# Kernel optimization log

Measured on AMD Instinct MI355X. Metric: run time of the kernel, lower is better.

## Reference

```python
import jax, jax.numpy as jnp
import numpy as np

K_CHAINS, N_STATES, ALPHABET, SEQ_LEN = 3, 12, 32, 64


def setup_inputs() -> dict:
    key = jax.random.key(0)
    k0, k1, k2, k3, k4 = jax.random.split(key, 5)
    return {
        "ys": jax.random.randint(k0, (SEQ_LEN,), 0, ALPHABET),
        "transition": jax.random.normal(k1, (K_CHAINS, N_STATES, N_STATES), jnp.float32),
        "emission": jax.random.normal(k2, (K_CHAINS, N_STATES, ALPHABET), jnp.float32),
        "choice": jax.random.normal(k3, (K_CHAINS,), jnp.float32),
        "prior": jax.random.normal(k4, (K_CHAINS, N_STATES), jnp.float32),
    }


def reference(ys, transition, emission, choice, prior):
    K, S = transition.shape[0], transition.shape[1]
    c = jax.nn.log_softmax(choice)                  # (K,)
    t = jax.nn.log_softmax(transition, axis=-1)     # (K,S,S)
    e = jax.nn.log_softmax(emission, axis=-1)       # (K,S,A)
    p = jax.nn.log_softmax(prior, axis=-1)          # (K,S)

    # enumerate expanded state space: tuples (s_1..s_K, i) -> N = S^K * K rows
    grids = jnp.meshgrid(*([jnp.arange(S)] * K + [jnp.arange(K)]), indexing="ij")
    tbl = jnp.stack(grids, -1).reshape(-1, K + 1)   # (N, K+1)
    states = tbl[:, :K]                             # (N, K) chain states
    chain = tbl[:, K]                               # (N,)   active chain index

    # transition matrix A[m, n] = logprob(old expanded state n -> new expanded state m)
    onehot = jax.nn.one_hot(chain, K, dtype=bool)   # (N, K)
    eq = states[:, None, :] == states[None, :, :]   # (N_new, N_old, K)
    valid = jnp.where(onehot[:, None, :], True, eq).all(-1)  # non-active chains unchanged
    s_new = jnp.take_along_axis(states, chain[:, None], axis=1)[:, 0]  # (N,) new state of active chain
    s_old = states[:, chain]                        # (N_old, N_new): old state at chain[m]
    t_term = t[chain[None, :], s_old, s_new[None, :]]  # (N_old, N_new)
    Amat = c[chain][:, None] + t_term.T + jnp.where(valid, 0.0, -jnp.inf)  # (N_new, N_old)

    # emission table B[m, y] = e[chain[m], state of active chain, y]
    B = e[chain, s_new]                             # (N, A)

    # initial alpha: sum_j p[j, s_j] + c[i]
    alpha0 = p[jnp.arange(K)[None, :], states].sum(-1) + c[chain]  # (N,)

    def step(alpha, y):
        alpha = B[:, y] + jax.nn.logsumexp(alpha[None, :] + Amat, axis=-1)
        return alpha, None

    alpha, _ = jax.lax.scan(step, alpha0, ys)
    return jax.nn.logsumexp(alpha)
```

## Files before the change

kernel.cpp:

```cpp
#include <hip/hip_runtime.h>
#include <math.h>

#define KC 3
#define S 12
#define SS 1728
#define AB 32
#define TLEN 64
#define NTHREADS 448
#define NWAVES 7
#define NSLICE 432
#define LN2F 0.69314718055994530942f

__global__ __launch_bounds__(NTHREADS, 2)
void hmm_fwd_kernel(const int* __restrict__ ys,
                    const float* __restrict__ transition,
                    const float* __restrict__ emission,
                    const float* __restrict__ choice,
                    const float* __restrict__ prior,
                    float* __restrict__ out)
{
    __shared__ __align__(16) float A[2][KC][SS];
    __shared__ __align__(16) float T_s[KC][S][S];
    __shared__ float EC[KC][S][AB];
    __shared__ float p_lin[KC][S];
    __shared__ float c_lin[KC];
    __shared__ int   ys_s[TLEN];
    __shared__ float wsum[NWAVES];

    const int tid = threadIdx.x;

    if (tid < TLEN) ys_s[tid] = ys[tid];

    if (tid == 0) {
        float m = fmaxf(fmaxf(choice[0], choice[1]), choice[2]);
        float e0 = __expf(choice[0]-m), e1 = __expf(choice[1]-m), e2 = __expf(choice[2]-m);
        float inv = 1.f / (e0+e1+e2);
        c_lin[0] = e0*inv; c_lin[1] = e1*inv; c_lin[2] = e2*inv;
    }
    if (tid >= 1 && tid < 1 + KC) {
        int k = tid - 1;
        float m = -INFINITY;
        #pragma unroll
        for (int i = 0; i < S; ++i) m = fmaxf(m, prior[k*S + i]);
        float ev[S]; float s = 0.f;
        #pragma unroll
        for (int i = 0; i < S; ++i) { ev[i] = __expf(prior[k*S + i] - m); s += ev[i]; }
        float inv = 1.f / s;
        #pragma unroll
        for (int i = 0; i < S; ++i) p_lin[k][i] = ev[i] * inv;
    }
    if (tid >= 64 && tid < 64 + KC*S) {
        int r = tid - 64;
        int k = r / S, i = r % S;
        const float* row = transition + (k*S + i)*S;
        float m = -INFINITY;
        #pragma unroll
        for (int j = 0; j < S; ++j) m = fmaxf(m, row[j]);
        float ev[S]; float s = 0.f;
        #pragma unroll
        for (int j = 0; j < S; ++j) { ev[j] = __expf(row[j] - m); s += ev[j]; }
        float inv = 1.f / s;
        #pragma unroll
        for (int j = 0; j < S; ++j) T_s[k][i][j] = ev[j] * inv;
    }
    if (tid >= 128 && tid < 128 + KC*S) {
        int r = tid - 128;
        int k = r / S, si = r % S;
        float cm = fmaxf(fmaxf(choice[0], choice[1]), choice[2]);
        float ce = __expf(choice[k]-cm) /
                   (__expf(choice[0]-cm) + __expf(choice[1]-cm) + __expf(choice[2]-cm));
        const float* row = emission + (k*S + si)*AB;
        float m = -INFINITY;
        #pragma unroll
        for (int a = 0; a < AB; ++a) m = fmaxf(m, row[a]);
        float ev[AB]; float s = 0.f;
        #pragma unroll
        for (int a = 0; a < AB; ++a) { ev[a] = __expf(row[a] - m); s += ev[a]; }
        float inv = ce / s;
        #pragma unroll
        for (int a = 0; a < AB; ++a) EC[k][si][a] = ev[a] * inv;
    }
    __syncthreads();

    const bool active = (tid < NSLICE);
    const int sk = tid / 144;
    const int q  = tid % 144;
    const int ka = (sk == 0) ? 1 : 0;
    const int kb = (sk == 2) ? 1 : 2;

    int base = 0, str = 0;
    float2 T2[S][6];
    float  own[S];
    int    off[S];

    if (active) {
        if (sk == 0)      { base = q;                   str = 144; }
        else if (sk == 1) { base = (q/12)*144 + (q%12); str = 12;  }
        else              { base = q*12;                str = 1;   }
        #pragma unroll
        for (int i = 0; i < S; ++i) off[i] = base + i*str;

        #pragma unroll
        for (int i = 0; i < S; ++i) {
            const float2* tr = reinterpret_cast<const float2*>(&T_s[sk][i][0]);
            #pragma unroll
            for (int m = 0; m < 6; ++m) T2[i][m] = tr[m];
        }

        const float pq = p_lin[ka == 1 ? 1 : 0][q/12] * 0.f +
                         p_lin[(sk==0)?1:0][q/12] * p_lin[(sk==2)?1:2][q%12];
        const float ck = c_lin[sk];
        #pragma unroll
        for (int i = 0; i < S; ++i) {
            float v = p_lin[sk][i] * pq * ck;
            own[i] = v;
            A[0][sk][off[i]] = v;
        }
    }
    __syncthreads();

    float logR = 0.f;
    float invR = 1.f;
    int cur = 0;

    for (int t = 0; t < TLEN; ++t) {
        const int y = ys_s[t];

        if (active) {
            float ecol[S];
            #pragma unroll
            for (int j = 0; j < S; ++j) ecol[j] = EC[sk][j][y];

            float beta[S];
            if (sk == 2) {
                const float4* pa = reinterpret_cast<const float4*>(&A[cur][0][base]);
                const float4* pb = reinterpret_cast<const float4*>(&A[cur][1][base]);
                #pragma unroll
                for (int m = 0; m < 3; ++m) {
                    float4 x = pa[m], z = pb[m];
                    beta[4*m+0] = own[4*m+0] + x.x + z.x;
                    beta[4*m+1] = own[4*m+1] + x.y + z.y;
                    beta[4*m+2] = own[4*m+2] + x.z + z.z;
                    beta[4*m+3] = own[4*m+3] + x.w + z.w;
                }
            } else {
                #pragma unroll
                for (int i = 0; i < S; ++i)
                    beta[i] = own[i] + A[cur][ka][off[i]] + A[cur][kb][off[i]];
            }

            float2 acc2[6];
            #pragma unroll
            for (int m = 0; m < 6; ++m) { acc2[m].x = 0.f; acc2[m].y = 0.f; }
            #pragma unroll
            for (int i = 0; i < S; ++i) {
                const float bv = beta[i];
                #pragma unroll
                for (int m = 0; m < 6; ++m) {
                    acc2[m].x += bv * T2[i][m].x;
                    acc2[m].y += bv * T2[i][m].y;
                }
            }

            #pragma unroll
            for (int j = 0; j < S; ++j) {
                float a = (j & 1) ? acc2[j>>1].y : acc2[j>>1].x;
                own[j] = a * ecol[j] * invR;
            }

            if (sk == 2) {
                float4* pw = reinterpret_cast<float4*>(&A[cur^1][2][base]);
                pw[0] = make_float4(own[0], own[1], own[2],  own[3]);
                pw[1] = make_float4(own[4], own[5], own[6],  own[7]);
                pw[2] = make_float4(own[8], own[9], own[10], own[11]);
            } else {
                #pragma unroll
                for (int j = 0; j < S; ++j) A[cur^1][sk][off[j]] = own[j];
            }
        }

        if ((t & 7) == 7) {
            float part = 0.f;
            if (active) {
                #pragma unroll
                for (int j = 0; j < S; ++j) part += own[j];
            }
            #pragma unroll
            for (int o = 32; o > 0; o >>= 1) part += __shfl_xor(part, o);
            if ((tid & 63) == 0) wsum[tid >> 6] = part;
        }
        __syncthreads();

        if ((t & 7) == 7 && t < TLEN-1) {
            float R = wsum[0];
            #pragma unroll
            for (int w = 1; w < NWAVES; ++w) R += wsum[w];
            invR = __builtin_amdgcn_rcpf(R);
            logR += __log2f(R);
        } else {
            invR = 1.f;
        }
        cur ^= 1;
    }

    if (tid == 0) {
        float R = wsum[0];
        #pragma unroll
        for (int w = 1; w < NWAVES; ++w) R += wsum[w];
        out[0] = LN2F * (__log2f(R) + logR);
    }
}

extern "C" void kernel_launch(void* const* d_in, const int* in_sizes, int n_in,
                              void* d_out, int out_size, void* d_ws, size_t ws_size,
                              hipStream_t stream) {
    const int*   ys         = (const int*)  d_in[0];
    const float* transition = (const float*)d_in[1];
    const float* emission   = (const float*)d_in[2];
    const float* choice     = (const float*)d_in[3];
    const float* prior      = (const float*)d_in[4];
    float* out = (float*)d_out;

    hipLaunchKernelGGL(hmm_fwd_kernel, dim3(1), dim3(NTHREADS), 0, stream,
                       ys, transition, emission, choice, prior, out);
}
```

Baseline: 72.55 us.

## Split forward step into beta-sum phase with swizzled shared layout

Restructures each time step into two phases. First, every thread sums the three chain slices of alpha into a shared beta buffer using float4 loads. After a barrier, each slice thread gathers its beta column through an XOR-swizzled address map meant to avoid LDS bank conflicts, and the emission table is transposed so each emission column is read as three float4 loads. The intent is to cut strided scattered LDS reads and redundant per-slice summation, at the cost of an extra __syncthreads per step and a single non-double-buffered alpha array whose in-place writes must stay race-free.

```diff
diff --git a/kernel.cpp b/kernel.cpp
--- a/kernel.cpp
+++ b/kernel.cpp
@@ -11,6 +11,13 @@
 #define NSLICE 432
 #define LN2F 0.69314718055994530942f
 
+__device__ __forceinline__ int swz_word(int n) {
+    int r   = n / 12;
+    int pos = n % 12;
+    int v = (((r & 1) << 2) | (pos >> 2)) ^ ((r >> 1) & 7);
+    return ((r >> 1) << 5) + (v << 2) + (pos & 3);
+}
+
 __global__ __launch_bounds__(NTHREADS, 2)
 void hmm_fwd_kernel(const int* __restrict__ ys,
                     const float* __restrict__ transition,
@@ -19,9 +26,10 @@
                     const float* __restrict__ prior,
                     float* __restrict__ out)
 {
-    __shared__ __align__(16) float A[2][KC][SS];
-    __shared__ __align__(16) float T_s[KC][S][S];
-    __shared__ float EC[KC][S][AB];
+    __shared__ __align__(16) float ABUF[5760];
+    __shared__ __align__(16) float BETA[2304];
+    __shared__ __align__(16) float ECt[KC*AB*S];
+    __shared__ float T_s[KC][S][S];
     __shared__ float p_lin[KC][S];
     __shared__ float c_lin[KC];
     __shared__ int   ys_s[TLEN];
@@ -65,11 +73,11 @@
     }
     if (tid >= 128 && tid < 128 + KC*S) {
         int r = tid - 128;
-        int k = r / S, si = r % S;
+        int k = r / S, sj = r % S;
         float cm = fmaxf(fmaxf(choice[0], choice[1]), choice[2]);
         float ce = __expf(choice[k]-cm) /
                    (__expf(choice[0]-cm) + __expf(choice[1]-cm) + __expf(choice[2]-cm));
-        const float* row = emission + (k*S + si)*AB;
+        const float* row = emission + (k*S + sj)*AB;
         float m = -INFINITY;
         #pragma unroll
         for (int a = 0; a < AB; ++a) m = fmaxf(m, row[a]);
@@ -78,112 +86,112 @@
         for (int a = 0; a < AB; ++a) { ev[a] = __expf(row[a] - m); s += ev[a]; }
         float inv = ce / s;
         #pragma unroll
-        for (int a = 0; a < AB; ++a) EC[k][si][a] = ev[a] * inv;
+        for (int a = 0; a < AB; ++a) ECt[(k*AB + a)*S + sj] = ev[a] * inv;
     }
     __syncthreads();
 
-    const bool active = (tid < NSLICE);
+    const bool active = tid < NSLICE;
     const int sk = tid / 144;
     const int q  = tid % 144;
-    const int ka = (sk == 0) ? 1 : 0;
-    const int kb = (sk == 2) ? 1 : 2;
-
-    int base = 0, str = 0;
-    float2 T2[S][6];
-    float  own[S];
-    int    off[S];
+
+    int rd[S], wr[S];
+    float4 T4[S][3];
 
     if (active) {
-        if (sk == 0)      { base = q;                   str = 144; }
-        else if (sk == 1) { base = (q/12)*144 + (q%12); str = 12;  }
-        else              { base = q*12;                str = 1;   }
-        #pragma unroll
-        for (int i = 0; i < S; ++i) off[i] = base + i*str;
+        int n[S];
+        if (sk == 0) {
+            #pragma unroll
+            for (int j = 0; j < S; ++j) n[j] = j*144 + q;
+        } else if (sk == 1) {
+            int b = (q/12)*144 + (q%12);
+            #pragma unroll
+            for (int j = 0; j < S; ++j) n[j] = b + j*12;
+        } else {
+            #pragma unroll
+            for (int j = 0; j < S; ++j) n[j] = q*12 + j;
+        }
+        #pragma unroll
+        for (int j = 0; j < S; ++j) rd[j] = swz_word(n[j]);
+        #pragma unroll
+        for (int j = 0; j < S; ++j)
+            wr[j] = (sk == 0) ? n[j] : (sk == 1 ? 1728 + n[j] : 3456 + swz_word(n[j]));
 
         #pragma unroll
         for (int i = 0; i < S; ++i) {
-            const float2* tr = reinterpret_cast<const float2*>(&T_s[sk][i][0]);
-            #pragma unroll
-            for (int m = 0; m < 6; ++m) T2[i][m] = tr[m];
-        }
-
-        const float pq = p_lin[ka == 1 ? 1 : 0][q/12] * 0.f +
-                         p_lin[(sk==0)?1:0][q/12] * p_lin[(sk==2)?1:2][q%12];
-        const float ck = c_lin[sk];
-        #pragma unroll
-        for (int i = 0; i < S; ++i) {
-            float v = p_lin[sk][i] * pq * ck;
-            own[i] = v;
-            A[0][sk][off[i]] = v;
-        }
-    }
+            #pragma unroll
+            for (int c = 0; c < 3; ++c) {
+                T4[i][c] = *reinterpret_cast<const float4*>(&T_s[sk][i][4*c]);
+                asm volatile("" : "+v"(T4[i][c].x), "+v"(T4[i][c].y),
+                                  "+v"(T4[i][c].z), "+v"(T4[i][c].w));
+            }
+        }
+
+        float pq = (sk == 0) ? p_lin[1][q/12] * p_lin[2][q%12]
+                 : (sk == 1) ? p_lin[0][q/12] * p_lin[2][q%12]
+                 :             p_lin[0][q/12] * p_lin[1][q%12];
+        float ck = c_lin[sk];
+        #pragma unroll
+        for (int j = 0; j < S; ++j) ABUF[wr[j]] = p_lin[sk][j] * pq * ck;
+    }
+    const int p13 = tid / 3, pm3 = tid % 3;
+    const int swzw = ((p13 >> 1) << 5) + ((((((p13 & 1) << 2) | pm3)) ^ ((p13 >> 1) & 7)) << 2);
     __syncthreads();
 
-    float logR = 0.f;
-    float invR = 1.f;
-    int cur = 0;
+    float logR = 0.f, invR = 1.f;
 
     for (int t = 0; t < TLEN; ++t) {
         const int y = ys_s[t];
+        float4 b4, e0, e1, e2;
 
         if (active) {
-            float ecol[S];
-            #pragma unroll
-            for (int j = 0; j < S; ++j) ecol[j] = EC[sk][j][y];
-
-            float beta[S];
-            if (sk == 2) {
-                const float4* pa = reinterpret_cast<const float4*>(&A[cur][0][base]);
-                const float4* pb = reinterpret_cast<const float4*>(&A[cur][1][base]);
-                #pragma unroll
-                for (int m = 0; m < 3; ++m) {
-                    float4 x = pa[m], z = pb[m];
-                    beta[4*m+0] = own[4*m+0] + x.x + z.x;
-                    beta[4*m+1] = own[4*m+1] + x.y + z.y;
-                    beta[4*m+2] = own[4*m+2] + x.z + z.z;
-                    beta[4*m+3] = own[4*m+3] + x.w + z.w;
-                }
-            } else {
-                #pragma unroll
-                for (int i = 0; i < S; ++i)
-                    beta[i] = own[i] + A[cur][ka][off[i]] + A[cur][kb][off[i]];
+            float4 a0 = *reinterpret_cast<const float4*>(&ABUF[4*tid]);
+            float4 a1 = *reinterpret_cast<const float4*>(&ABUF[1728 + 4*tid]);
+            float4 a2 = *reinterpret_cast<const float4*>(&ABUF[3456 + swzw]);
+            b4.x = a0.x + a1.x + a2.x;
+            b4.y = a0.y + a1.y + a2.y;
+            b4.z = a0.z + a1.z + a2.z;
+            b4.w = a0.w + a1.w + a2.w;
+            *reinterpret_cast<float4*>(&BETA[swzw]) = b4;
+            const float* eb = &ECt[(sk*AB + y)*S];
+            e0 = *reinterpret_cast<const float4*>(&eb[0]);
+            e1 = *reinterpret_cast<const float4*>(&eb[4]);
+            e2 = *reinterpret_cast<const float4*>(&eb[8]);
+        }
+        __syncthreads();
+
+        float4 o0, o1, o2;
+        if (active) {
+            float bv[S];
+            #pragma unroll
+            for (int i = 0; i < S; ++i) bv[i] = BETA[rd[i]];
+
+            float4 acc0 = {0,0,0,0}, acc1 = {0,0,0,0}, acc2 = {0,0,0,0};
+            #pragma unroll
+            for (int i = 0; i < S; ++i) {
+                const float b = bv[i];
+                acc0.x += b*T4[i][0].x; acc0.y += b*T4[i][0].y;
+                acc0.z += b*T4[i][0].z; acc0.w += b*T4[i][0].w;
+                acc1.x += b*T4[i][1].x; acc1.y += b*T4[i][1].y;
+                acc1.z += b*T4[i][1].z; acc1.w += b*T4[i][1].w;
+                acc2.x += b*T4[i][2].x; acc2.y += b*T4[i][2].y;
+                acc2.z += b*T4[i][2].z; acc2.w += b*T4[i][2].w;
             }
-
-            float2 acc2[6];
-            #pragma unroll
-            for (int m = 0; m < 6; ++m) { acc2[m].x = 0.f; acc2[m].y = 0.f; }
-            #pragma unroll
-            for (int i = 0; i < S; ++i) {
-                const float bv = beta[i];
-                #pragma unroll
-                for (int m = 0; m < 6; ++m) {
-                    acc2[m].x += bv * T2[i][m].x;
-                    acc2[m].y += bv * T2[i][m].y;
-                }
-            }
-
-            #pragma unroll
-            for (int j = 0; j < S; ++j) {
-                float a = (j & 1) ? acc2[j>>1].y : acc2[j>>1].x;
-                own[j] = a * ecol[j] * invR;
-            }
-
-            if (sk == 2) {
-                float4* pw = reinterpret_cast<float4*>(&A[cur^1][2][base]);
-                pw[0] = make_float4(own[0], own[1], own[2],  own[3]);
-                pw[1] = make_float4(own[4], own[5], own[6],  own[7]);
-                pw[2] = make_float4(own[8], own[9], own[10], own[11]);
-            } else {
-                #pragma unroll
-                for (int j = 0; j < S; ++j) A[cur^1][sk][off[j]] = own[j];
-            }
+            o0.x = acc0.x*e0.x*invR; o0.y = acc0.y*e0.y*invR;
+            o0.z = acc0.z*e0.z*invR; o0.w = acc0.w*e0.w*invR;
+            o1.x = acc1.x*e1.x*invR; o1.y = acc1.y*e1.y*invR;
+            o1.z = acc1.z*e1.z*invR; o1.w = acc1.w*e1.w*invR;
+            o2.x = acc2.x*e2.x*invR; o2.y = acc2.y*e2.y*invR;
+            o2.z = acc2.z*e2.z*invR; o2.w = acc2.w*e2.w*invR;
+
+            ABUF[wr[0]]  = o0.x; ABUF[wr[1]]  = o0.y; ABUF[wr[2]]  = o0.z; ABUF[wr[3]]  = o0.w;
+            ABUF[wr[4]]  = o1.x; ABUF[wr[5]]  = o1.y; ABUF[wr[6]]  = o1.z; ABUF[wr[7]]  = o1.w;
+            ABUF[wr[8]]  = o2.x; ABUF[wr[9]]  = o2.y; ABUF[wr[10]] = o2.z; ABUF[wr[11]] = o2.w;
         }
 
         if ((t & 7) == 7) {
             float part = 0.f;
             if (active) {
-                #pragma unroll
-                for (int j = 0; j < S; ++j) part += own[j];
+                part = (o0.x+o0.y+o0.z+o0.w) + (o1.x+o1.y+o1.z+o1.w) + (o2.x+o2.y+o2.z+o2.w);
             }
             #pragma unroll
             for (int o = 32; o > 0; o >>= 1) part += __shfl_xor(part, o);
@@ -200,7 +208,6 @@
         } else {
             invR = 1.f;
         }
-        cur ^= 1;
     }
 
     if (tid == 0) {
```

Measured after the change: 65.46 us. 9.8% less time.
